# Kernel optimization log

Hardware: AMD Instinct MI355X
Metric: run time of the kernel (lower is better)

## Reference

```python
import jax, jax.numpy as jnp
import numpy as np

PI = float(np.pi)


def _lsa_cols(cost):
    """Jonker-Volgenant / Hungarian on a square cost matrix (numpy float64).
    Returns col_ind such that (arange(n), col_ind) is the optimal assignment,
    matching scipy.optimize.linear_sum_assignment for a square matrix."""
    n = cost.shape[0]
    C = np.zeros((n + 1, n + 1), dtype=np.float64)
    C[1:, 1:] = cost
    u = np.zeros(n + 1)
    v = np.zeros(n + 1)
    p = np.zeros(n + 1, dtype=np.int64)  # p[j] = row matched to column j (1-indexed)
    for i in range(1, n + 1):
        p[0] = i
        j0 = 0
        minv = np.full(n + 1, np.inf)
        way = np.zeros(n + 1, dtype=np.int64)
        used = np.zeros(n + 1, dtype=bool)
        while True:
            used[j0] = True
            i0 = p[j0]
            cur = C[i0] - u[i0] - v
            upd = (~used) & (cur < minv)
            minv = np.where(upd, cur, minv)
            way[upd] = j0
            masked = np.where(used, np.inf, minv)
            j1 = int(np.argmin(masked))
            delta = masked[j1]
            u[p[used]] += delta
            v[used] -= delta
            minv[~used] -= delta
            j0 = j1
            if p[j0] == 0:
                break
        while j0:
            j1 = way[j0]
            p[j0] = p[j1]
            j0 = j1
    col_to_row = p[1:] - 1  # row assigned to each column
    col_ind = np.empty(n, dtype=np.int64)
    col_ind[col_to_row] = np.arange(n)
    return col_ind


def _batched_assignment(input, target):
    # cdist p=2 : (B, N, N)
    diff = input[:, :, None, :] - target[:, None, :, :]
    cost = jnp.sqrt(jnp.sum(diff * diff, axis=-1))
    cost_np = np.asarray(cost, dtype=np.float64)
    # serial per-sample Hungarian solve (mirrors the original scipy loop)
    cols = np.stack([_lsa_cols(cost_np[b]) for b in range(cost_np.shape[0])], axis=0)
    return jnp.asarray(cols)  # (B, N)


def setup_inputs() -> dict:
    key = jax.random.key(0)
    k1, k2 = jax.random.split(key)
    B, N, D = 128, 128, 5
    return {
        "input": jax.random.normal(k1, (B, N, D), dtype=jnp.float32),
        "target": jax.random.normal(k2, (B, N, D), dtype=jnp.float32),
    }


def reference(input, target):
    cols = _batched_assignment(input, target)  # (B, N), constant w.r.t. grads
    # row_ind is identity (square matrix), so aligned_pred == input;
    # aligned_true = target gathered by the optimal columns.
    aligned_true = jnp.take_along_axis(target, cols[:, :, None], axis=1)
    d = input - aligned_true
    x_loss = jnp.mean(d[..., 0] ** 2)
    y_loss = jnp.mean(d[..., 1] ** 2)
    E_loss = jnp.mean(d[..., 2] ** 2)
    theta_loss = jnp.mean(d[..., 3] ** 2)
    phi_diff = jnp.remainder(d[..., 4] + PI, 2.0 * PI) - PI  # wrap to (-pi, pi]
    phi_loss = jnp.mean(phi_diff ** 2)
    total_loss = x_loss + y_loss + E_loss + theta_loss + phi_loss
    # [total, x, y, E, theta, phi]
    return jnp.stack([total_loss, x_loss, y_loss, E_loss, theta_loss, phi_loss])
```

## Files before the change

kernel.cpp:

```cpp
#include <hip/hip_runtime.h>

#define NN 128
#define NB 128
#define ND 5
#define INFV 3.4028235e38f

__device__ __forceinline__ float wrap_phi(float x) {
  const float PI_F   = 3.14159265358979323846f;
  const float TWO_PI = 6.28318530717958647692f;
  float t = x + PI_F;
  float w = t - floorf(t * (1.0f / TWO_PI)) * TWO_PI;
  return w - PI_F;
}

#define DPP_SRC_INF(x, ctrl, rmask)                                           \
  __int_as_float(__builtin_amdgcn_update_dpp(                                 \
      0x7f800000, __float_as_int(x), (ctrl), (rmask), 0xF, false))

#define DPP_MIN_STEP(x, ctrl, rmask) x = fminf(x, DPP_SRC_INF(x, ctrl, rmask))

#define DPP_MIN2_STEP(x1, x2, ctrl, rmask)                                    \
  { float _a1 = DPP_SRC_INF(x1, ctrl, rmask);                                 \
    float _a2 = DPP_SRC_INF(x2, ctrl, rmask);                                 \
    float _t  = fmaxf(x1, _a1);                                               \
    x1 = fminf(x1, _a1);                                                      \
    x2 = fminf(fminf(x2, _a2), _t); }

__device__ __forceinline__ int rl_i(int v, int lane) {
  return __builtin_amdgcn_readlane(v, lane);
}
__device__ __forceinline__ float rl_f(float v, int lane) {
  return __int_as_float(__builtin_amdgcn_readlane(__float_as_int(v), lane));
}

__device__ __forceinline__ float wave_min_bcast(float x) {
  DPP_MIN_STEP(x, 0xB1,  0xF);
  DPP_MIN_STEP(x, 0x4E,  0xF);
  DPP_MIN_STEP(x, 0x141, 0xF);
  DPP_MIN_STEP(x, 0x140, 0xF);
  DPP_MIN_STEP(x, 0x142, 0xA);
  DPP_MIN_STEP(x, 0x143, 0xC);
  return rl_f(x, 63);
}

__device__ __forceinline__ void wave_min2_bcast(float &x1, float &x2) {
  DPP_MIN2_STEP(x1, x2, 0xB1,  0xF);
  DPP_MIN2_STEP(x1, x2, 0x4E,  0xF);
  DPP_MIN2_STEP(x1, x2, 0x141, 0xF);
  DPP_MIN2_STEP(x1, x2, 0x140, 0xF);
  DPP_MIN2_STEP(x1, x2, 0x142, 0xA);
  DPP_MIN2_STEP(x1, x2, 0x143, 0xC);
  x1 = rl_f(x1, 63);
  x2 = rl_f(x2, 63);
}

__global__ __launch_bounds__(64) void set2set_hungarian(
    const float* __restrict__ inp, const float* __restrict__ tgt,
    float* __restrict__ sums)
{
  const int b = blockIdx.x;
  const int lane = threadIdx.x;

  __shared__ __align__(16) float Csh[NN * NN];
  __shared__ float inpS[NN * ND];
  __shared__ int   rowOwner[NN + 1];
  __shared__ float uFree[NN + 1];

  const float* inB = inp + (size_t)b * NN * ND;
  const float* tgB = tgt + (size_t)b * NN * ND;

  for (int idx = lane; idx < NN * ND; idx += 64) inpS[idx] = inB[idx];
  for (int idx = lane; idx <= NN; idx += 64) { rowOwner[idx] = 0x7fffffff; uFree[idx] = 0.f; }
  __syncthreads();

  const int jA = 2 * lane;
  const int jB = 2 * lane + 1;
  const int c1A = jA + 1, c1B = jB + 1;

  float tA[ND], tB[ND];
  #pragma unroll
  for (int d = 0; d < ND; ++d) { tA[d] = tgB[jA * ND + d]; tB[d] = tgB[jB * ND + d]; }

  float vA = INFV, vB = INFV;
  int   rmA = 1,  rmB = 1;
  #pragma unroll 4
  for (int i = 0; i < NN; ++i) {
    float sA = 0.f, sB = 0.f;
    #pragma unroll
    for (int d = 0; d < ND; ++d) {
      float x = inpS[i * ND + d];
      float da = x - tA[d]; sA = fmaf(da, da, sA);
      float db = x - tB[d]; sB = fmaf(db, db, sB);
    }
    float cA = sqrtf(sA), cB = sqrtf(sB);
    ((float2*)(Csh + i * NN))[lane] = make_float2(cA, cB);
    if (cA < vA) { vA = cA; rmA = i + 1; }
    if (cB < vB) { vB = cB; rmB = i + 1; }
  }
  __syncthreads();

  atomicMin(&rowOwner[rmA], c1A);
  atomicMin(&rowOwner[rmB], c1B);
  __syncthreads();

  int   pA = (rowOwner[rmA] == c1A) ? rmA : 0;
  int   pB = (rowOwner[rmB] == c1B) ? rmB : 0;
  float uA = 0.f, uB = 0.f;
  int   wayA = 0, wayB = 0;

  unsigned long long remLo = __ballot(rowOwner[1 + lane]  == 0x7fffffff);
  unsigned long long remHi = __ballot(rowOwner[65 + lane] == 0x7fffffff);
  unsigned long long dijLo = 0ull, dijHi = 0ull;

  while (remLo | remHi) {
    int i;
    if (remLo) { int t = __ffsll(remLo) - 1; remLo &= remLo - 1ull; i = t + 1; }
    else       { int t = __ffsll(remHi) - 1; remHi &= remHi - 1ull; i = t + 65; }

    const float2 c = ((const float2*)(Csh + (i - 1) * NN))[lane];
    float rcA = c.x - vA, rcB = c.y - vB;
    float m1 = fminf(rcA, rcB), m2 = fmaxf(rcA, rcB);
    wave_min2_bcast(m1, m2);

    unsigned long long mA1 = __ballot(rcA == m1);
    unsigned long long mB1 = __ballot(rcB == m1);
    int l = __ffsll(mA1 | mB1) - 1;
    bool aside = (mA1 >> l) & 1ull;
    int owner = l;
    int slot = aside ? 0 : 1;

    int   pSel = slot ? pB : pA;
    float uSel = slot ? uB : uA;
    int   i0   = rl_i(pSel, owner);
    float uOld = rl_f(uSel, owner);

    float dv = m2 - m1;
    bool selA = (lane == owner) && (slot == 0);
    bool selB = (lane == owner) && (slot == 1);
    vA -= selA ? dv : 0.f;   vB -= selB ? dv : 0.f;
    pA  = selA ? i  : pA;    pB  = selB ? i  : pB;
    uA  = selA ? m2 : uA;    uB  = selB ? m2 : uB;

    if (i0 != 0) {
      if (lane == 0) uFree[i0] = uOld;
      if (i0 <= 64) dijLo |= 1ull << (i0 - 1);
      else          dijHi |= 1ull << (i0 - 65);
    }
  }

  while (dijLo | dijHi) {
    int i;
    if (dijLo) { int t = __ffsll(dijLo) - 1; dijLo &= dijLo - 1ull; i = t + 1; }
    else       { int t = __ffsll(dijHi) - 1; dijHi &= dijHi - 1ull; i = t + 65; }
    float uf = uFree[i];

    float mA = INFV, mB = INFV;
    bool usedA = false, usedB = false;
    float ucur = uf;
    int   j0 = 0, i0 = i;
    float ui0 = uf;
    int   jfree = 0;

    for (int guard = 0; guard <= NN + 1; ++guard) {
      usedA |= (j0 == c1A);
      usedB |= (j0 == c1B);
      const float2 c = ((const float2*)(Csh + (i0 - 1) * NN))[lane];
      float curA = c.x - ui0 - vA;
      float curB = c.y - ui0 - vB;
      bool updA = !usedA && (curA < mA);
      bool updB = !usedB && (curB < mB);
      mA = updA ? curA : mA;  wayA = updA ? j0 : wayA;
      mB = updB ? curB : mB;  wayB = updB ? j0 : wayB;

      float x = fminf(usedA ? INFV : mA, usedB ? INFV : mB);
      float delta = wave_min_bcast(x);

      unsigned long long mskA = __ballot(!usedA && (mA == delta));
      unsigned long long mskB = __ballot(!usedB && (mB == delta));
      unsigned long long msk  = mskA | mskB;
      int l = __ffsll(msk) - 1;
      bool aside = (mskA >> l) & 1ull;
      int owner = l;
      int slot  = aside ? 0 : 1;
      int j1 = 2 * l + 1 + slot;

      ucur += delta;
      float dA = usedA ? delta : 0.f;
      float dB = usedB ? delta : 0.f;
      vA -= dA; uA += dA; mA -= (delta - dA);
      vB -= dB; uB += dB; mB -= (delta - dB);

      int   pSel = slot ? pB : pA;
      float uSel = slot ? uB : uA;
      int pj1 = rl_i(pSel, owner);
      if (pj1 == 0) { jfree = j1; break; }
      ui0 = rl_f(uSel, owner);
      j0 = j1; i0 = pj1;
    }

    int jj = jfree;
    for (int g = 0; g < NN + 1 && jj != 0; ++g) {
      int owner = (jj - 1) >> 1, slot = (jj - 1) & 1;
      int wSel = slot ? rl_i(wayB, owner) : rl_i(wayA, owner);
      int wj = wSel;
      int pnew; float unew;
      if (wj == 0) { pnew = i; unew = ucur; }
      else {
        int o2 = (wj - 1) >> 1, s2 = (wj - 1) & 1;
        int   pS2 = s2 ? rl_i(pB, o2) : rl_i(pA, o2);
        float uS2 = s2 ? rl_f(uB, o2) : rl_f(uA, o2);
        pnew = pS2; unew = uS2;
      }
      bool selA = (lane == owner) && (slot == 0);
      bool selB = (lane == owner) && (slot == 1);
      pA = selA ? pnew : pA;  uA = selA ? unew : uA;
      pB = selB ? pnew : pB;  uB = selB ? unew : uB;
      jj = wj;
    }
  }

  int rA = pA - 1;
  int rB = pB - 1;
  float acc[ND];
  #pragma unroll
  for (int d = 0; d < ND; ++d) {
    float dA = inpS[rA * ND + d] - tA[d];
    float dB = inpS[rB * ND + d] - tB[d];
    if (d == 4) { dA = wrap_phi(dA); dB = wrap_phi(dB); }
    acc[d] = dA * dA + dB * dB;
  }
  #pragma unroll
  for (int d = 0; d < ND; ++d) {
    float s = acc[d];
    #pragma unroll
    for (int off = 32; off > 0; off >>= 1) s += __shfl_xor(s, off);
    if (lane == 0) atomicAdd(&sums[d], s);
  }
}

__global__ void set2set_finalize(const float* __restrict__ sums, float* __restrict__ out) {
  const float inv = 1.0f / (128.0f * 128.0f);
  float x  = sums[0] * inv;
  float y  = sums[1] * inv;
  float E  = sums[2] * inv;
  float th = sums[3] * inv;
  float ph = sums[4] * inv;
  out[1] = x; out[2] = y; out[3] = E; out[4] = th; out[5] = ph;
  out[0] = x + y + E + th + ph;
}

extern "C" void kernel_launch(void* const* d_in, const int* in_sizes, int n_in,
                              void* d_out, int out_size, void* d_ws, size_t ws_size,
                              hipStream_t stream) {
  const float* inp = (const float*)d_in[0];
  const float* tgt = (const float*)d_in[1];
  float* out  = (float*)d_out;
  float* sums = (float*)d_ws;

  hipMemsetAsync(sums, 0, ND * sizeof(float), stream);
  set2set_hungarian<<<dim3(NB), dim3(64), 0, stream>>>(inp, tgt, sums);
  set2set_finalize<<<dim3(1), dim3(1), 0, stream>>>(sums, out);
}
```

Baseline: 462.8 us.

## Add reduction-transfer step and second augmenting row-reduction pass to Hungarian init

Adds a reduction-transfer phase after column reduction that sets u and tightens v for each matched column, following the Jonker-Volgenant initialisation. It then runs augmenting row reduction twice instead of once, feeding the rows displaced in the first pass into a second pass. The aim is to leave fewer free rows for the expensive serial Dijkstra augmentation. It also simplifies argmin selection to one ballot plus a readlane of the candidate column per iteration, at the cost of the extra init passes.

```diff
diff --git a/kernel.cpp b/kernel.cpp
--- a/kernel.cpp
+++ b/kernel.cpp
@@ -108,45 +108,70 @@
   float uA = 0.f, uB = 0.f;
   int   wayA = 0, wayB = 0;
 
+  {
+    unsigned long long mtA = __ballot(pA != 0);
+    unsigned long long mtB = __ballot(pB != 0);
+    while (mtA | mtB) {
+      int l, slot;
+      if (mtA) { l = __ffsll(mtA) - 1; mtA &= mtA - 1ull; slot = 0; }
+      else     { l = __ffsll(mtB) - 1; mtB &= mtB - 1ull; slot = 1; }
+      int owner = l;
+      int i = rl_i(slot ? pB : pA, owner);
+      const float2 c = ((const float2*)(Csh + (i - 1) * NN))[lane];
+      float rA_ = c.x - vA, rB_ = c.y - vB;
+      if (lane == owner) { if (slot) rB_ = INFV; else rA_ = INFV; }
+      float mu = wave_min_bcast(fminf(rA_, rB_));
+      bool selA = (lane == owner) && (slot == 0);
+      bool selB = (lane == owner) && (slot == 1);
+      vA -= selA ? mu : 0.f;   vB -= selB ? mu : 0.f;
+      uA  = selA ? mu : uA;    uB  = selB ? mu : uB;
+    }
+  }
+
   unsigned long long remLo = __ballot(rowOwner[1 + lane]  == 0x7fffffff);
   unsigned long long remHi = __ballot(rowOwner[65 + lane] == 0x7fffffff);
   unsigned long long dijLo = 0ull, dijHi = 0ull;
 
-  while (remLo | remHi) {
-    int i;
-    if (remLo) { int t = __ffsll(remLo) - 1; remLo &= remLo - 1ull; i = t + 1; }
-    else       { int t = __ffsll(remHi) - 1; remHi &= remHi - 1ull; i = t + 65; }
-
-    const float2 c = ((const float2*)(Csh + (i - 1) * NN))[lane];
-    float rcA = c.x - vA, rcB = c.y - vB;
-    float m1 = fminf(rcA, rcB), m2 = fmaxf(rcA, rcB);
-    wave_min2_bcast(m1, m2);
-
-    unsigned long long mA1 = __ballot(rcA == m1);
-    unsigned long long mB1 = __ballot(rcB == m1);
-    int l = __ffsll(mA1 | mB1) - 1;
-    bool aside = (mA1 >> l) & 1ull;
-    int owner = l;
-    int slot = aside ? 0 : 1;
-
-    int   pSel = slot ? pB : pA;
-    float uSel = slot ? uB : uA;
-    int   i0   = rl_i(pSel, owner);
-    float uOld = rl_f(uSel, owner);
-
-    float dv = m2 - m1;
-    bool selA = (lane == owner) && (slot == 0);
-    bool selB = (lane == owner) && (slot == 1);
-    vA -= selA ? dv : 0.f;   vB -= selB ? dv : 0.f;
-    pA  = selA ? i  : pA;    pB  = selB ? i  : pB;
-    uA  = selA ? m2 : uA;    uB  = selB ? m2 : uB;
-
-    if (i0 != 0) {
-      if (lane == 0) uFree[i0] = uOld;
-      if (i0 <= 64) dijLo |= 1ull << (i0 - 1);
-      else          dijHi |= 1ull << (i0 - 65);
-    }
-  }
+  #pragma unroll 1
+  for (int pass = 0; pass < 2; ++pass) {
+    unsigned long long inLo = remLo, inHi = remHi;
+    unsigned long long outLo = 0ull, outHi = 0ull;
+    while (inLo | inHi) {
+      int i;
+      if (inLo) { int t = __ffsll(inLo) - 1; inLo &= inLo - 1ull; i = t + 1; }
+      else      { int t = __ffsll(inHi) - 1; inHi &= inHi - 1ull; i = t + 65; }
+
+      const float2 c = ((const float2*)(Csh + (i - 1) * NN))[lane];
+      float rcA = c.x - vA, rcB = c.y - vB;
+      float m1 = fminf(rcA, rcB), m2 = fmaxf(rcA, rcB);
+      float candv = m1;
+      int   candc = (rcA <= rcB) ? c1A : c1B;
+      wave_min2_bcast(m1, m2);
+
+      unsigned long long msk = __ballot(candv == m1);
+      int l = __ffsll(msk) - 1;
+      int j1 = rl_i(candc, l);
+      int owner = l, slot = (j1 - 1) & 1;
+
+      int   i0   = rl_i(slot ? pB : pA, owner);
+      float uOld = rl_f(slot ? uB : uA, owner);
+
+      float dv = m2 - m1;
+      bool selA = (lane == owner) && (slot == 0);
+      bool selB = (lane == owner) && (slot == 1);
+      vA -= selA ? dv : 0.f;   vB -= selB ? dv : 0.f;
+      pA  = selA ? i  : pA;    pB  = selB ? i  : pB;
+      uA  = selA ? m2 : uA;    uB  = selB ? m2 : uB;
+
+      if (i0 != 0) {
+        if (lane == 0) uFree[i0] = uOld;
+        if (i0 <= 64) outLo |= 1ull << (i0 - 1);
+        else          outHi |= 1ull << (i0 - 65);
+      }
+    }
+    remLo = outLo; remHi = outHi;
+  }
+  dijLo = remLo; dijHi = remHi;
 
   while (dijLo | dijHi) {
     int i;
@@ -172,17 +197,15 @@
       mA = updA ? curA : mA;  wayA = updA ? j0 : wayA;
       mB = updB ? curB : mB;  wayB = updB ? j0 : wayB;
 
-      float x = fminf(usedA ? INFV : mA, usedB ? INFV : mB);
-      float delta = wave_min_bcast(x);
-
-      unsigned long long mskA = __ballot(!usedA && (mA == delta));
-      unsigned long long mskB = __ballot(!usedB && (mB == delta));
-      unsigned long long msk  = mskA | mskB;
+      float mAx = usedA ? INFV : mA;
+      float mBx = usedB ? INFV : mB;
+      float candv = fminf(mAx, mBx);
+      int   candc = (mAx <= mBx) ? c1A : c1B;
+      float delta = wave_min_bcast(candv);
+      unsigned long long msk = __ballot(candv == delta);
       int l = __ffsll(msk) - 1;
-      bool aside = (mskA >> l) & 1ull;
-      int owner = l;
-      int slot  = aside ? 0 : 1;
-      int j1 = 2 * l + 1 + slot;
+      int j1 = rl_i(candc, l);
+      int owner = l, slot = (j1 - 1) & 1;
 
       ucur += delta;
       float dA = usedA ? delta : 0.f;
@@ -190,26 +213,22 @@
       vA -= dA; uA += dA; mA -= (delta - dA);
       vB -= dB; uB += dB; mB -= (delta - dB);
 
-      int   pSel = slot ? pB : pA;
-      float uSel = slot ? uB : uA;
-      int pj1 = rl_i(pSel, owner);
+      int pj1 = rl_i(slot ? pB : pA, owner);
       if (pj1 == 0) { jfree = j1; break; }
-      ui0 = rl_f(uSel, owner);
+      ui0 = rl_f(slot ? uB : uA, owner);
       j0 = j1; i0 = pj1;
     }
 
     int jj = jfree;
     for (int g = 0; g < NN + 1 && jj != 0; ++g) {
       int owner = (jj - 1) >> 1, slot = (jj - 1) & 1;
-      int wSel = slot ? rl_i(wayB, owner) : rl_i(wayA, owner);
-      int wj = wSel;
+      int wj = slot ? rl_i(wayB, owner) : rl_i(wayA, owner);
       int pnew; float unew;
       if (wj == 0) { pnew = i; unew = ucur; }
       else {
         int o2 = (wj - 1) >> 1, s2 = (wj - 1) & 1;
-        int   pS2 = s2 ? rl_i(pB, o2) : rl_i(pA, o2);
-        float uS2 = s2 ? rl_f(uB, o2) : rl_f(uA, o2);
-        pnew = pS2; unew = uS2;
+        pnew = s2 ? rl_i(pB, o2) : rl_i(pA, o2);
+        unew = s2 ? rl_f(uB, o2) : rl_f(uA, o2);
       }
       bool selA = (lane == owner) && (slot == 0);
       bool selB = (lane == owner) && (slot == 1);
```

Measured after the change: 402.3 us. 1.15x faster.
